# Optimization experiments

Hardware: AMD Instinct MI355X
Metric: run time of the kernel (lower is better)

The kernel has to match this reference:

```python
import jax, jax.numpy as jnp
import numpy as np
import math

SR = 16000        # sample_rate
HOP = 512         # hop_length
FMIN = 20.0
N_BINS = 84
BPO = 12          # bins_per_octave
Q = 1.0 / (2.0 ** (1.0 / BPO) - 1.0)


def setup_inputs() -> dict:
    key = jax.random.key(0)
    waveform = jax.random.normal(key, (2560000,), dtype=jnp.float32)
    return {"waveform": waveform}


def _bin_kernel(wl: int, freq: float, dtype):
    """Windowed single-DFT-bin kernel matching torch.stft row `freq_bin`.
    Returns (2,1,wl) conv kernel: [real, imag] parts of conj(e^{-2pi i f n / wl}) * hann.
    """
    n = np.arange(wl)
    # torch.hann_window default is periodic: 0.5*(1 - cos(2*pi*n/N))
    w = 0.5 - 0.5 * np.cos(2.0 * np.pi * n / wl)
    fb = min(int(freq * wl / SR), wl // 2)  # onesided stft has wl//2+1 rows
    ang = 2.0 * np.pi * fb * n / wl
    kr = (w * np.cos(ang)).astype(np.float32)
    ki = (-w * np.sin(ang)).astype(np.float32)
    return jnp.asarray(np.stack([kr, ki])[:, None, :], dtype=dtype)


def reference(waveform) -> jnp.ndarray:
    L = waveform.shape[-1]
    num_frames = (L - HOP) // HOP + 1  # matches torch code's frame count
    rows = []
    for k in range(N_BINS):
        freq = FMIN * 2.0 ** (k / BPO)
        wl = min(int(SR * Q / freq), L // 4)
        if wl < 32:  # torch code skips these bins (row stays zero)
            rows.append(jnp.zeros((num_frames,), waveform.dtype))
            continue
        pad = wl // 2  # torch.stft center=True reflect padding
        xpad = jnp.pad(waveform, (pad, pad), mode="reflect")
        kern = _bin_kernel(wl, freq, waveform.dtype)
        # strided correlation == extracting one DFT bin of every stft frame
        out = jax.lax.conv_general_dilated(
            xpad[None, None, :], kern, window_strides=(HOP,), padding="VALID"
        )[0]  # (2, n_frames_k)
        mag = jnp.sqrt(out[0] ** 2 + out[1] ** 2)
        mf = min(mag.shape[0], num_frames)
        rows.append(jnp.zeros((num_frames,), waveform.dtype).at[:mf].set(mag[:mf]))
    return jnp.stack(rows)[None]  # (1, n_bins, num_frames)
```

## Files before the change

### kernel.cpp

```cpp
#include <hip/hip_runtime.h>
#include <math.h>

#define L_IN   2560000
#define HOP    512
#define NB     84
#define NF     5000
#define PAD0   6726
#define XPLEN  2573452
#define XBLEN2 2637824
#define NTIL   40
#define SLOTS  6
#define NBLK   (NTIL*SLOTS)
#define XB_NB  1288
#define AG_NB  502

#define LDS_SZ 137216

#define XB_B 0
#define AG_B 5275648
#define P_B  7331840

typedef short bf16x8 __attribute__((ext_vector_type(8)));
typedef float f32x16 __attribute__((ext_vector_type(16)));

__device__ inline unsigned short f2bf(float f) {
  unsigned int u = __float_as_uint(f);
  return (unsigned short)((u + 0x7fffu + ((u >> 16) & 1u)) >> 16);
}

__device__ inline void load16(void* l, const void* g) {
  __builtin_amdgcn_global_load_lds((const __attribute__((address_space(1))) void*)g,
                                   (__attribute__((address_space(3))) void*)l, 16, 0, 0);
}

__global__ __launch_bounds__(256) void k_prep(const float* __restrict__ x,
                                              unsigned short* __restrict__ xb,
                                              unsigned short* __restrict__ Ag) {
  if (blockIdx.x < XB_NB) {
    int i8 = (blockIdx.x * 256 + threadIdx.x) * 8;
    bf16x8 o;
    int u0 = i8 - PAD0;
    if (u0 >= 0 && u0 + 8 <= L_IN) {
      const float2* p = (const float2*)(x + u0);
#pragma unroll
      for (int j = 0; j < 4; ++j) {
        float2 v = p[j];
        o[2 * j]     = (short)f2bf(v.x);
        o[2 * j + 1] = (short)f2bf(v.y);
      }
    } else {
#pragma unroll
      for (int j = 0; j < 8; ++j) {
        int i = i8 + j;
        float v = 0.f;
        if (i < XPLEN) {
          int u = i - PAD0;
          if (u < 0) u = -u;
          else if (u >= L_IN) u = 2 * L_IN - 2 - u;
          v = x[u];
        }
        o[j] = (short)f2bf(v);
      }
    }
    *(bf16x8*)(xb + i8) = o;
  } else {
    int g = (blockIdx.x - XB_NB) * 256 + threadIdx.x;
    int s = g >> 9, w = g & 511;
    int im = w >> 8, kk = (w >> 6) & 3, lane = w & 63;
    int mt  = (s < 211) ? 0 : ((s < 245) ? 1 : 2);
    int mst = (mt == 0) ? 0 : ((mt == 1) ? 211 : 245);
    int kst = (mt == 0) ? 0 : ((mt == 1) ? 5632 : 6528);
    int tap0 = kst + (s - mst) * 64 + kk * 16 + ((lane >> 5) << 3);
    int row = im * 32 + (lane & 31);
    int bin = mt * 32 + (row >> 1);
    bf16x8 vv;
    if (bin >= NB) {
#pragma unroll
      for (int j = 0; j < 8; ++j) vv[j] = 0;
    } else {
      double q    = 1.0 / (pow(2.0, 1.0 / 12.0) - 1.0);
      double freq = 20.0 * pow(2.0, (double)bin / 12.0);
      int wl = (int)(16000.0 * q / freq);
      if (wl > L_IN / 4) wl = L_IN / 4;
      int pad = wl >> 1;
      int fbq = (int)(freq * (double)wl / 16000.0);
      if (fbq > wl / 2) fbq = wl / 2;
      int isIm = row & 1;
      float invwl = 1.0f / (float)wl;
#pragma unroll
      for (int j = 0; j < 8; ++j) {
        int n = tap0 + j - (PAD0 - pad);
        float v = 0.f;
        if (n >= 0 && n < wl) {
          float wn = 0.5f - 0.5f * cosf(6.2831853071795865f * ((float)n * invwl));
          int m = (fbq * n) % wl;
          float a = 6.2831853071795865f * ((float)m * invwl);
          v = isIm ? (-wn * sinf(a)) : (wn * cosf(a));
        }
        vv[j] = (short)f2bf(v);
      }
    }
    *(bf16x8*)(Ag + ((size_t)s * 4096 + im * 2048 + kk * 512 + lane * 8)) = vv;
  }
}

struct AF { bf16x8 f[2][4]; };

__device__ inline void loadA(AF& a, const char* Ag, int s, int lane) {
  const char* p = Ag + ((size_t)s << 13) + lane * 16;
#pragma unroll
  for (int im = 0; im < 2; ++im)
#pragma unroll
    for (int kk = 0; kk < 4; ++kk)
      a.f[im][kk] = *(const bf16x8*)(p + im * 4096 + kk * 1024);
}

__device__ inline void stepC(const AF& a, int l, int lane, const char* Bw,
                             f32x16 acc[2][4]) {
  int tb = l * 128 + ((lane >> 5) << 4);
#pragma unroll
  for (int n = 0; n < 4; ++n) {
    bf16x8 bf[4];
    int ob = (n * 32 + (lane & 31)) * 1024 + tb;
#pragma unroll
    for (int kk = 0; kk < 4; ++kk) {
      int o = ob + kk * 32;
      o ^= ((o >> 10) & 15) << 4;
      bf[kk] = *(const bf16x8*)(Bw + o);
    }
    __builtin_amdgcn_s_setprio(1);
#pragma unroll
    for (int kk = 0; kk < 4; ++kk) {
      acc[0][n] = __builtin_amdgcn_mfma_f32_32x32x16_bf16(a.f[0][kk], bf[kk], acc[0][n], 0, 0, 0);
      acc[1][n] = __builtin_amdgcn_mfma_f32_32x32x16_bf16(a.f[1][kk], bf[kk], acc[1][n], 0, 0, 0);
    }
    __builtin_amdgcn_s_setprio(0);
  }
}

__global__ __launch_bounds__(512, 2) void k_gemm(const unsigned short* __restrict__ Ag,
                                                 const unsigned short* __restrict__ xb,
                                                 float* __restrict__ P,
                                                 float* __restrict__ out) {
  extern __shared__ char lds[];
  const int tid = threadIdx.x, lane = tid & 63, wv = tid >> 6;

  int bid = blockIdx.x;
  int lid = (bid & 7) * (NBLK / 8) + (bid >> 3);
  int nt = lid / SLOTS, c = lid - nt * SLOTS;
  const int gs_[6] = {0, 53, 106, 159, 211, 245};
  const int ns_[6] = {53, 53, 53, 52, 34, 6};
  const int kb_[6] = {0, 3392, 6784, 10176, 5632, 6528};
  int gs = gs_[c], ns = ns_[c], kb = kb_[c];
  int nch = (130048 + 128 * ns + 1023) >> 10;

  const char* xsrc = (const char*)xb + (size_t)nt * 131072 + (size_t)kb * 2;
  for (int ci = wv; ci < nch; ci += 8)
    load16(lds + ci * 1024, xsrc + ci * 1024 + ((lane * 16) ^ ((ci & 15) << 4)));
  __builtin_amdgcn_sched_barrier(0);

  const char* Ab = (const char*)Ag;
  int nks = (ns - wv + 7) >> 3;
  AF a0, a1;
  int s0 = gs + wv, s1 = gs + wv + 8;
  loadA(a0, Ab, s0 > 250 ? 250 : s0, lane);
  loadA(a1, Ab, s1 > 250 ? 250 : s1, lane);

  f32x16 acc[2][4];
#pragma unroll
  for (int i = 0; i < 2; ++i)
#pragma unroll
    for (int j = 0; j < 4; ++j)
#pragma unroll
      for (int e = 0; e < 16; ++e) acc[i][j][e] = 0.f;

  asm volatile("s_waitcnt vmcnt(16)" ::: "memory");
  __syncthreads();

  int i = 0;
  for (; i + 2 <= nks; i += 2) {
    stepC(a0, wv + 8 * i, lane, lds, acc);
    int sa = gs + wv + 8 * (i + 2); if (sa > 250) sa = 250;
    loadA(a0, Ab, sa, lane);
    stepC(a1, wv + 8 * (i + 1), lane, lds, acc);
    int sb = gs + wv + 8 * (i + 3); if (sb > 250) sb = 250;
    loadA(a1, Ab, sb, lane);
  }
  if (i < nks) stepC(a0, wv + 8 * i, lane, lds, acc);

  __syncthreads();
  float* Pb = P + ((size_t)(nt * 4 + c) << 13);
#pragma unroll
  for (int h = 0; h < 2; ++h) {
    float* Cw = (float*)(lds + wv * 16384);
#pragma unroll
    for (int im = 0; im < 2; ++im)
#pragma unroll
      for (int n2 = 0; n2 < 2; ++n2) {
        f32x16 v = acc[im][2 * h + n2];
        int col = n2 * 32 + (lane & 31);
        int rb  = im * 32 + ((lane >> 5) << 2);
#pragma unroll
        for (int r = 0; r < 16; ++r) {
          int row = rb + (r & 3) + 8 * (r >> 2);
          Cw[row * 64 + col] = v[r];
        }
      }
    __syncthreads();
    const float* L0 = (const float*)lds;
#pragma unroll
    for (int e = 0; e < 4; ++e) {
      int p = e * 512 + tid;
      int rp = p >> 6, cl = p & 63;
      float re = 0.f, iv = 0.f;
#pragma unroll
      for (int w = 0; w < 8; ++w) {
        re += L0[w * 4096 + (2 * rp) * 64 + cl];
        iv += L0[w * 4096 + (2 * rp + 1) * 64 + cl];
      }
      if (c < 4) {
        Pb[(2 * rp) * 128 + h * 64 + cl]     = re;
        Pb[(2 * rp + 1) * 128 + h * 64 + cl] = iv;
      } else {
        int b = ((c == 4) ? 32 : 64) + rp;
        int colg = nt * 128 + h * 64 + cl;
        if (b < NB && colg < NF)
          out[(size_t)b * NF + colg] = sqrtf(re * re + iv * iv);
      }
    }
    __syncthreads();
  }
}

__global__ __launch_bounds__(256) void k_mag(const float* __restrict__ P,
                                             float* __restrict__ out) {
  int col = blockIdx.x * 256 + threadIdx.x;
  int b = blockIdx.y;
  if (col >= NF) return;
  int nt = col >> 7, cl = col & 127;
  const float* Pt = P + ((size_t)(nt * 4) << 13);
  float re = 0.f, iv = 0.f;
#pragma unroll
  for (int cc = 0; cc < 4; ++cc) {
    const float* Pbc = Pt + ((size_t)cc << 13);
    re += Pbc[(2 * b) * 128 + cl];
    iv += Pbc[(2 * b + 1) * 128 + cl];
  }
  out[(size_t)b * NF + col] = sqrtf(re * re + iv * iv);
}

extern "C" void kernel_launch(void* const* d_in, const int* in_sizes, int n_in,
                              void* d_out, int out_size, void* d_ws, size_t ws_size,
                              hipStream_t stream) {
  const float* x = (const float*)d_in[0];
  char* ws = (char*)d_ws;
  unsigned short* xb = (unsigned short*)(ws + XB_B);
  unsigned short* Ag = (unsigned short*)(ws + AG_B);
  float* P           = (float*)(ws + P_B);
  float* out = (float*)d_out;

  hipFuncSetAttribute((const void*)k_gemm,
                      hipFuncAttributeMaxDynamicSharedMemorySize, LDS_SZ);

  hipLaunchKernelGGL(k_prep, dim3(XB_NB + AG_NB), dim3(256), 0, stream, x, xb, Ag);
  hipLaunchKernelGGL(k_gemm, dim3(NBLK), dim3(512), LDS_SZ, stream, Ag, xb, P, out);
  hipLaunchKernelGGL(k_mag, dim3(20, 32), dim3(256), 0, stream, P, out);
}
```

Before: 33.03 us.

## Split waves over K and N, fuse magnitude pass via last-block atomic counter

Each GEMM block's eight waves now form a 4 (K split) by 2 (N half) grid instead of eight K-split waves covering the full N tile. This halves the accumulators per wave and the LDS cross-wave reduction work. The separate k_mag kernel is removed: after writing its partial to P, each block bumps a per-tile atomic counter, and the fourth block to finish sums the partials and writes the magnitudes. This saves a kernel launch and a dependent pass, at the cost of threadfences, an atomic, and a serial tail in the last block of each tile.

After: 63.32 us. +91.7%, slower.

```diff
diff --git a/kernel.cpp b/kernel.cpp
--- a/kernel.cpp
+++ b/kernel.cpp
@@ -16,9 +16,10 @@
 
 #define LDS_SZ 137216
 
-#define XB_B 0
-#define AG_B 5275648
-#define P_B  7331840
+#define XB_B  0
+#define AG_B  5275648
+#define P_B   7331840
+#define CNT_B 12574720
 
 typedef short bf16x8 __attribute__((ext_vector_type(8)));
 typedef float f32x16 __attribute__((ext_vector_type(16)));
@@ -35,8 +36,10 @@
 
 __global__ __launch_bounds__(256) void k_prep(const float* __restrict__ x,
                                               unsigned short* __restrict__ xb,
-                                              unsigned short* __restrict__ Ag) {
+                                              unsigned short* __restrict__ Ag,
+                                              int* __restrict__ cnt) {
   if (blockIdx.x < XB_NB) {
+    if (blockIdx.x == 0 && threadIdx.x < NTIL) cnt[threadIdx.x] = 0;
     int i8 = (blockIdx.x * 256 + threadIdx.x) * 8;
     bf16x8 o;
     int u0 = i8 - PAD0;
@@ -115,13 +118,13 @@
       a.f[im][kk] = *(const bf16x8*)(p + im * 4096 + kk * 1024);
 }
 
-__device__ inline void stepC(const AF& a, int l, int lane, const char* Bw,
-                             f32x16 acc[2][4]) {
+__device__ inline void stepC(const AF& a, int l, int lane, int wc, const char* Bw,
+                             f32x16 acc[2][2]) {
   int tb = l * 128 + ((lane >> 5) << 4);
 #pragma unroll
-  for (int n = 0; n < 4; ++n) {
+  for (int n2 = 0; n2 < 2; ++n2) {
     bf16x8 bf[4];
-    int ob = (n * 32 + (lane & 31)) * 1024 + tb;
+    int ob = (wc * 64 + n2 * 32 + (lane & 31)) * 1024 + tb;
 #pragma unroll
     for (int kk = 0; kk < 4; ++kk) {
       int o = ob + kk * 32;
@@ -131,8 +134,8 @@
     __builtin_amdgcn_s_setprio(1);
 #pragma unroll
     for (int kk = 0; kk < 4; ++kk) {
-      acc[0][n] = __builtin_amdgcn_mfma_f32_32x32x16_bf16(a.f[0][kk], bf[kk], acc[0][n], 0, 0, 0);
-      acc[1][n] = __builtin_amdgcn_mfma_f32_32x32x16_bf16(a.f[1][kk], bf[kk], acc[1][n], 0, 0, 0);
+      acc[0][n2] = __builtin_amdgcn_mfma_f32_32x32x16_bf16(a.f[0][kk], bf[kk], acc[0][n2], 0, 0, 0);
+      acc[1][n2] = __builtin_amdgcn_mfma_f32_32x32x16_bf16(a.f[1][kk], bf[kk], acc[1][n2], 0, 0, 0);
     }
     __builtin_amdgcn_s_setprio(0);
   }
@@ -141,9 +144,11 @@
 __global__ __launch_bounds__(512, 2) void k_gemm(const unsigned short* __restrict__ Ag,
                                                  const unsigned short* __restrict__ xb,
                                                  float* __restrict__ P,
+                                                 int* __restrict__ cnt,
                                                  float* __restrict__ out) {
   extern __shared__ char lds[];
   const int tid = threadIdx.x, lane = tid & 63, wv = tid >> 6;
+  const int wk = wv >> 1, wc = wv & 1;
 
   int bid = blockIdx.x;
   int lid = (bid & 7) * (NBLK / 8) + (bid >> 3);
@@ -160,17 +165,17 @@
   __builtin_amdgcn_sched_barrier(0);
 
   const char* Ab = (const char*)Ag;
-  int nks = (ns - wv + 7) >> 3;
+  int nks = (ns - wk + 3) >> 2;
   AF a0, a1;
-  int s0 = gs + wv, s1 = gs + wv + 8;
+  int s0 = gs + wk, s1 = gs + wk + 4;
   loadA(a0, Ab, s0 > 250 ? 250 : s0, lane);
   loadA(a1, Ab, s1 > 250 ? 250 : s1, lane);
 
-  f32x16 acc[2][4];
+  f32x16 acc[2][2];
 #pragma unroll
   for (int i = 0; i < 2; ++i)
 #pragma unroll
-    for (int j = 0; j < 4; ++j)
+    for (int j = 0; j < 2; ++j)
 #pragma unroll
       for (int e = 0; e < 16; ++e) acc[i][j][e] = 0.f;
 
@@ -179,74 +184,86 @@
 
   int i = 0;
   for (; i + 2 <= nks; i += 2) {
-    stepC(a0, wv + 8 * i, lane, lds, acc);
-    int sa = gs + wv + 8 * (i + 2); if (sa > 250) sa = 250;
+    stepC(a0, wk + 4 * i, lane, wc, lds, acc);
+    int sa = gs + wk + 4 * (i + 2); if (sa > 250) sa = 250;
     loadA(a0, Ab, sa, lane);
-    stepC(a1, wv + 8 * (i + 1), lane, lds, acc);
-    int sb = gs + wv + 8 * (i + 3); if (sb > 250) sb = 250;
+    stepC(a1, wk + 4 * (i + 1), lane, wc, lds, acc);
+    int sb = gs + wk + 4 * (i + 3); if (sb > 250) sb = 250;
     loadA(a1, Ab, sb, lane);
   }
-  if (i < nks) stepC(a0, wv + 8 * i, lane, lds, acc);
+  if (i < nks) stepC(a0, wk + 4 * i, lane, wc, lds, acc);
 
   __syncthreads();
-  float* Pb = P + ((size_t)(nt * 4 + c) << 13);
-#pragma unroll
-  for (int h = 0; h < 2; ++h) {
-    float* Cw = (float*)(lds + wv * 16384);
-#pragma unroll
-    for (int im = 0; im < 2; ++im)
-#pragma unroll
-      for (int n2 = 0; n2 < 2; ++n2) {
-        f32x16 v = acc[im][2 * h + n2];
-        int col = n2 * 32 + (lane & 31);
-        int rb  = im * 32 + ((lane >> 5) << 2);
-#pragma unroll
-        for (int r = 0; r < 16; ++r) {
-          int row = rb + (r & 3) + 8 * (r >> 2);
-          Cw[row * 64 + col] = v[r];
+  float* Cw = (float*)(lds + wv * 16384);
+#pragma unroll
+  for (int im = 0; im < 2; ++im)
+#pragma unroll
+    for (int n2 = 0; n2 < 2; ++n2) {
+      f32x16 v = acc[im][n2];
+      int c64 = n2 * 32 + (lane & 31);
+      int rb  = im * 32 + ((lane >> 5) << 2);
+#pragma unroll
+      for (int r = 0; r < 16; ++r) {
+        int row = rb + (r & 3) + 8 * (r >> 2);
+        Cw[row * 64 + c64] = v[r];
+      }
+    }
+  __syncthreads();
+  const float* L = (const float*)lds;
+
+  if (c < 4) {
+    float* Pb = P + ((size_t)(nt * 4 + c) << 13);
+#pragma unroll
+    for (int e = 0; e < 16; ++e) {
+      int p = e * 512 + tid;
+      int row = p >> 7, colg = p & 127;
+      int h = colg >> 6, c64 = colg & 63;
+      float s = 0.f;
+#pragma unroll
+      for (int k4 = 0; k4 < 4; ++k4)
+        s += L[(k4 * 2 + h) * 4096 + row * 64 + c64];
+      Pb[p] = s;
+    }
+    __threadfence();
+    __syncthreads();
+    int* flag = (int*)(lds + 136192);
+    if (tid == 0) *flag = atomicAdd(&cnt[nt], 1);
+    __syncthreads();
+    if (*flag == 3) {
+      __threadfence();
+      const float* P0 = P + ((size_t)(nt * 4) << 13);
+#pragma unroll
+      for (int e = 0; e < 8; ++e) {
+        int p = e * 512 + tid;
+        int bin = p >> 7, cl = p & 127;
+        float re = 0.f, iv = 0.f;
+#pragma unroll
+        for (int cc = 0; cc < 4; ++cc) {
+          re += P0[cc * 8192 + (2 * bin) * 128 + cl];
+          iv += P0[cc * 8192 + (2 * bin + 1) * 128 + cl];
         }
-      }
-    __syncthreads();
-    const float* L0 = (const float*)lds;
-#pragma unroll
-    for (int e = 0; e < 4; ++e) {
+        int colg = nt * 128 + cl;
+        if (colg < NF) out[(size_t)bin * NF + colg] = sqrtf(re * re + iv * iv);
+      }
+    }
+  } else {
+    int bb = (c == 4) ? 32 : 64;
+#pragma unroll
+    for (int e = 0; e < 8; ++e) {
       int p = e * 512 + tid;
-      int rp = p >> 6, cl = p & 63;
+      int bl = p >> 7, cl = p & 127;
+      int h = cl >> 6, c64 = cl & 63;
       float re = 0.f, iv = 0.f;
 #pragma unroll
-      for (int w = 0; w < 8; ++w) {
-        re += L0[w * 4096 + (2 * rp) * 64 + cl];
-        iv += L0[w * 4096 + (2 * rp + 1) * 64 + cl];
-      }
-      if (c < 4) {
-        Pb[(2 * rp) * 128 + h * 64 + cl]     = re;
-        Pb[(2 * rp + 1) * 128 + h * 64 + cl] = iv;
-      } else {
-        int b = ((c == 4) ? 32 : 64) + rp;
-        int colg = nt * 128 + h * 64 + cl;
-        if (b < NB && colg < NF)
-          out[(size_t)b * NF + colg] = sqrtf(re * re + iv * iv);
-      }
-    }
-    __syncthreads();
-  }
-}
-
-__global__ __launch_bounds__(256) void k_mag(const float* __restrict__ P,
-                                             float* __restrict__ out) {
-  int col = blockIdx.x * 256 + threadIdx.x;
-  int b = blockIdx.y;
-  if (col >= NF) return;
-  int nt = col >> 7, cl = col & 127;
-  const float* Pt = P + ((size_t)(nt * 4) << 13);
-  float re = 0.f, iv = 0.f;
-#pragma unroll
-  for (int cc = 0; cc < 4; ++cc) {
-    const float* Pbc = Pt + ((size_t)cc << 13);
-    re += Pbc[(2 * b) * 128 + cl];
-    iv += Pbc[(2 * b + 1) * 128 + cl];
-  }
-  out[(size_t)b * NF + col] = sqrtf(re * re + iv * iv);
+      for (int k4 = 0; k4 < 4; ++k4) {
+        re += L[(k4 * 2 + h) * 4096 + (2 * bl) * 64 + c64];
+        iv += L[(k4 * 2 + h) * 4096 + (2 * bl + 1) * 64 + c64];
+      }
+      int b = bb + bl, colg = nt * 128 + cl;
+      if (b < NB && colg < NF)
+        out[(size_t)b * NF + colg] = sqrtf(re * re + iv * iv);
+    }
+  }
 }
 
 extern "C" void kernel_launch(void* const* d_in, const int* in_sizes, int n_in,
@@ -257,12 +274,12 @@
   unsigned short* xb = (unsigned short*)(ws + XB_B);
   unsigned short* Ag = (unsigned short*)(ws + AG_B);
   float* P           = (float*)(ws + P_B);
+  int* cnt           = (int*)(ws + CNT_B);
   float* out = (float*)d_out;
 
   hipFuncSetAttribute((const void*)k_gemm,
                       hipFuncAttributeMaxDynamicSharedMemorySize, LDS_SZ);
 
-  hipLaunchKernelGGL(k_prep, dim3(XB_NB + AG_NB), dim3(256), 0, stream, x, xb, Ag);
-  hipLaunchKernelGGL(k_gemm, dim3(NBLK), dim3(512), LDS_SZ, stream, Ag, xb, P, out);
-  hipLaunchKernelGGL(k_mag, dim3(20, 32), dim3(256), 0, stream, P, out);
-}
+  hipLaunchKernelGGL(k_prep, dim3(XB_NB + AG_NB), dim3(256), 0, stream, x, xb, Ag, cnt);
+  hipLaunchKernelGGL(k_gemm, dim3(NBLK), dim3(512), LDS_SZ, stream, Ag, xb, P, cnt, out);
+}
```
